# Kernel tuning notes

Hardware: AMD Instinct MI355X
Metric: run time of the kernel (lower is better)

## Reference

```python
import jax, jax.numpy as jnp
import numpy as np

T = 64          # temporal frames folded into batch: B = b * T
DIM = 64        # base_channel
V = 25          # num_point (skeleton joints)
NSTEP = 3       # n_step -> time_steps = arange(NSTEP+1)
CLIPS = 256     # b = N * M clips
B = CLIPS * T   # 16384
LEAK = 0.01     # nn.LeakyReLU default negative_slope


def _init_pe(length, d_model):
    # sinusoidal PE, identical to ODEFunc.init_pe
    pos = np.arange(length, dtype=np.float32)[:, None]
    div = np.exp(np.arange(0, d_model, 2, dtype=np.float32) * (-np.log(10000.0) / d_model))
    pe = np.zeros((length, d_model), dtype=np.float32)
    pe[:, 0::2] = np.sin(pos * div)
    pe[:, 1::2] = np.cos(pos * div)
    return jnp.asarray(pe)


def setup_inputs() -> dict:
    key = jax.random.key(0)
    ks = jax.random.split(key, 8)
    first_point = jax.random.normal(ks[0], (B, DIM, V), dtype=jnp.float32)
    # row-normalized random adjacency (stand-in for Graph.A_norm)
    A = jax.random.uniform(ks[1], (V, V), dtype=jnp.float32)
    A = A / jnp.sum(A, axis=1, keepdims=True)
    scale = 0.05
    W1 = jax.random.normal(ks[2], (DIM, DIM), dtype=jnp.float32) * scale
    b1 = jax.random.normal(ks[3], (DIM,), dtype=jnp.float32) * scale
    W2 = jax.random.normal(ks[4], (DIM, DIM), dtype=jnp.float32) * scale
    b2 = jax.random.normal(ks[5], (DIM,), dtype=jnp.float32) * scale
    Wp = jax.random.normal(ks[6], (DIM, DIM), dtype=jnp.float32) * scale
    bp = jax.random.normal(ks[7], (DIM,), dtype=jnp.float32) * scale
    temporal_pe = _init_pe(T + NSTEP, DIM)  # (T+N, dim) buffer
    time_steps = jnp.arange(NSTEP + 1, dtype=jnp.float32)
    return {"first_point": first_point, "time_steps": time_steps,
            "A": A, "W1": W1, "b1": b1, "W2": W2, "b2": b2,
            "Wp": Wp, "bp": bp, "temporal_pe": temporal_pe}


def reference(first_point, time_steps, A, W1, b1, W2, b2, Wp, bp, temporal_pe):
    Bn = first_point.shape[0]
    b = Bn // T

    def conv1x1(x, W, bb):  # Conv1d(dim, dim, 1): x (n, c, v)
        return jnp.einsum('oc,ncv->nov', W, x) + bb[None, :, None]

    def lrelu(x):
        return jnp.where(x >= 0, x, LEAK * x)

    def ode_func(t, x):
        # add_pe: pe rows [int(t), int(t)+T) added per-frame
        ti = jnp.floor(t).astype(jnp.int32)
        pe = jax.lax.dynamic_slice(temporal_pe, (ti, 0), (T, DIM))  # (T, dim)
        x = (x.reshape(b, T, DIM, V) + pe[None, :, :, None]).reshape(Bn, DIM, V)
        x = jnp.einsum('vu,ncu->ncv', A, x)
        x = lrelu(conv1x1(x, W1, b1))
        x = jnp.einsum('vu,ncu->ncv', A, x)
        x = lrelu(conv1x1(x, W2, b2))
        return conv1x1(x, Wp, bp)

    def rk4_step(y, t0_dt):  # torchdiffeq 'rk4' = 3/8-rule (rk4_alt_step_func)
        t0, dt = t0_dt
        k1 = ode_func(t0, y)
        k2 = ode_func(t0 + dt / 3, y + dt * k1 / 3)
        k3 = ode_func(t0 + 2 * dt / 3, y + dt * (k2 - k1 / 3))
        k4 = ode_func(t0 + dt, y + dt * (k1 - k2 + k3))
        y1 = y + dt * (k1 + 3 * (k2 + k3) + k4) / 8
        return y1, y1

    t0s = time_steps[:-1]
    dts = time_steps[1:] - time_steps[:-1]
    _, ys = jax.lax.scan(rk4_step, first_point, (t0s, dts))
    return jnp.concatenate([first_point[None], ys], axis=0)  # (NSTEP+1, B, C, V)
```

## Files before the change

kernel.cpp:

```cpp
#include <hip/hip_runtime.h>
#include <math.h>

#define DIMC 64
#define V25  25
#define NSTEP 3
#define BTOT 16384
#define LEAK 0.01f

typedef _Float16 half8  __attribute__((ext_vector_type(8)));
typedef _Float16 half4v __attribute__((ext_vector_type(4)));
typedef float    float4v __attribute__((ext_vector_type(4)));

#define MFMA16x16x32F16 __builtin_amdgcn_mfma_f32_16x16x32_f16

#define CV_STRIDE 36
#define VC_STRIDE 72
#define W_STRIDE  72

__device__ __forceinline__ int clampi03(int x) {
    return x < 0 ? 0 : (x > 3 ? 3 : x);
}

__launch_bounds__(256, 2)
__global__ void sode_kernel(const float* __restrict__ fp,
                            const float* __restrict__ ts,
                            const float* __restrict__ Ag,
                            const float* __restrict__ W1g, const float* __restrict__ b1g,
                            const float* __restrict__ W2g, const float* __restrict__ b2g,
                            const float* __restrict__ Wpg, const float* __restrict__ bpg,
                            const float* __restrict__ peg,
                            float* __restrict__ out)
{
    __shared__ __align__(16) _Float16 Wl[3*64*W_STRIDE];
    __shared__ __align__(16) _Float16 bufcv[4*64*CV_STRIDE];
    __shared__ __align__(16) _Float16 bufvc[4*32*VC_STRIDE];

    const int tid  = threadIdx.x;
    const int lane = tid & 63;
    const int wid  = tid >> 6;
    const int m    = lane & 15;
    const int q    = lane >> 4;
    const int n    = blockIdx.x * 4 + wid;
    const int tmod = n & 63;

    for (int idx = tid; idx < 64*64; idx += 256) {
        int o = idx >> 6, c = idx & 63;
        int d = o*W_STRIDE + c;
        Wl[d]                 = (_Float16)W1g[idx];
        Wl[64*W_STRIDE + d]   = (_Float16)W2g[idx];
        Wl[2*64*W_STRIDE + d] = (_Float16)Wpg[idx];
    }
    __syncthreads();

    _Float16* bcv = bufcv + wid * 64 * CV_STRIDE;
    _Float16* bvc = bufvc + wid * 32 * VC_STRIDE;

    half8 BA[2];
    for (int nt = 0; nt < 2; ++nt) {
        int v = 16*nt + m;
        for (int j = 0; j < 8; ++j) {
            int u = 8*q + j;
            BA[nt][j] = (v < V25 && u < V25) ? (_Float16)Ag[v*V25 + u] : (_Float16)0.f;
        }
    }

    float4v Y[4][2], Acc[4][2], D[4][2], kreg[4][2];
    for (int mt = 0; mt < 4; ++mt)
      for (int nt = 0; nt < 2; ++nt) {
        float4v y;
        int v = 16*nt + m;
        for (int r = 0; r < 4; ++r) {
            int c = 16*mt + 4*q + r;
            y[r] = (v < V25) ? fp[(size_t)n*1600 + c*25 + v] : 0.f;
        }
        Y[mt][nt] = y;
      }

    const float4v z4 = {0.f, 0.f, 0.f, 0.f};

    auto stage = [&](int ti, auto&& fxn) {
        const float* perow = peg + (ti + tmod) * 64;
        for (int mt = 0; mt < 4; ++mt) {
            float pv[4];
            for (int r = 0; r < 4; ++r) pv[r] = perow[16*mt + 4*q + r];
            for (int nt = 0; nt < 2; ++nt) {
                int v = 16*nt + m;
                for (int r = 0; r < 4; ++r)
                    bcv[(16*mt + 4*q + r)*CV_STRIDE + v] = (_Float16)(fxn(mt, nt, r) + pv[r]);
            }
        }
    };

    auto amix = [&]() {
        half8 af[4];
        for (int mt = 0; mt < 4; ++mt) {
            const half4v* p = (const half4v*)(bcv + (16*mt + m)*CV_STRIDE + 8*q);
            half4v lo = p[0], hi = p[1];
            half8 a;
            for (int j = 0; j < 4; ++j) { a[j] = lo[j]; a[4+j] = hi[j]; }
            af[mt] = a;
        }
        float4v acc[4][2];
        for (int mt = 0; mt < 4; ++mt)
          for (int nt = 0; nt < 2; ++nt)
            acc[mt][nt] = MFMA16x16x32F16(af[mt], BA[nt], z4, 0, 0, 0);
        for (int mt = 0; mt < 4; ++mt)
          for (int nt = 0; nt < 2; ++nt) {
            half4v h;
            for (int r = 0; r < 4; ++r) h[r] = (_Float16)acc[mt][nt][r];
            *(half4v*)(bvc + (16*nt + m)*VC_STRIDE + 16*mt + 4*q) = h;
          }
    };

    auto conv = [&](const _Float16* Wbase, const float* bias, bool act, int dst) {
        half8 bf[2][2];
        for (int nt = 0; nt < 2; ++nt)
          for (int ks = 0; ks < 2; ++ks)
            bf[nt][ks] = *(const half8*)(bvc + (16*nt + m)*VC_STRIDE + 32*ks + 8*q);
        float4v acc[4][2];
        for (int mt = 0; mt < 4; ++mt) {
            const _Float16* wr = Wbase + (16*mt + m)*W_STRIDE + 8*q;
            half8 w0 = *(const half8*)(wr);
            half8 w1 = *(const half8*)(wr + 32);
            for (int nt = 0; nt < 2; ++nt) {
                float4v a = MFMA16x16x32F16(w0, bf[nt][0], z4, 0, 0, 0);
                acc[mt][nt] = MFMA16x16x32F16(w1, bf[nt][1], a, 0, 0, 0);
            }
        }
        for (int mt = 0; mt < 4; ++mt) {
            float bv[4];
            for (int r = 0; r < 4; ++r) bv[r] = bias[16*mt + 4*q + r];
            for (int nt = 0; nt < 2; ++nt) {
                float4v a = acc[mt][nt];
                for (int r = 0; r < 4; ++r) {
                    float x = a[r] + bv[r];
                    if (act) x = (x >= 0.f) ? x : LEAK * x;
                    a[r] = x;
                }
                if (dst == 2) {
                    kreg[mt][nt] = a;
                } else if (dst == 1) {
                    half4v h;
                    for (int r = 0; r < 4; ++r) h[r] = (_Float16)a[r];
                    *(half4v*)(bvc + (16*nt + m)*VC_STRIDE + 16*mt + 4*q) = h;
                } else {
                    int v = 16*nt + m;
                    for (int r = 0; r < 4; ++r)
                        bcv[(16*mt + 4*q + r)*CV_STRIDE + v] = (_Float16)a[r];
                }
            }
        }
    };

    auto feval = [&]() {
        amix();
        conv(Wl,                 b1g, true,  0);
        amix();
        conv(Wl +   64*W_STRIDE, b2g, true,  1);
        conv(Wl + 2*64*W_STRIDE, bpg, false, 2);
    };

    auto store_Y = [&](int step) {
        float* op = out + (size_t)step * BTOT * 1600 + (size_t)n * 1600;
        for (int mt = 0; mt < 4; ++mt)
          for (int nt = 0; nt < 2; ++nt) {
            int v = 16*nt + m;
            if (v < V25)
                for (int r = 0; r < 4; ++r)
                    op[(16*mt + 4*q + r)*25 + v] = Y[mt][nt][r];
          }
    };

    store_Y(0);

    float tsr[4];
    for (int i = 0; i < 4; ++i) tsr[i] = ts[i];

#pragma unroll 1
    for (int st = 0; st < NSTEP; ++st) {
        float t0 = tsr[st];
        float dt = tsr[st+1] - t0;
        float dt3 = dt * (1.f/3.f);
        int ti1 = clampi03((int)floorf(t0));
        int ti2 = clampi03((int)floorf(t0 + dt3));
        int ti3 = clampi03((int)floorf(t0 + 2.f*dt3));
        int ti4 = clampi03((int)floorf(t0 + dt));

        stage(ti1, [&](int mt, int nt, int r) { return Y[mt][nt][r]; });
        feval();
        for (int mt = 0; mt < 4; ++mt)
          for (int nt = 0; nt < 2; ++nt) { Acc[mt][nt] = kreg[mt][nt]; D[mt][nt] = kreg[mt][nt]; }
        stage(ti2, [&](int mt, int nt, int r) { return Y[mt][nt][r] + dt3 * kreg[mt][nt][r]; });

        feval();
        stage(ti3, [&](int mt, int nt, int r) {
            return Y[mt][nt][r] + dt * kreg[mt][nt][r] - dt3 * Acc[mt][nt][r];
        });
        for (int mt = 0; mt < 4; ++mt)
          for (int nt = 0; nt < 2; ++nt)
            for (int r = 0; r < 4; ++r) {
                float kk = kreg[mt][nt][r];
                Acc[mt][nt][r] += 3.f * kk;
                D[mt][nt][r]   -= kk;
            }

        feval();
        stage(ti4, [&](int mt, int nt, int r) {
            return Y[mt][nt][r] + dt * (D[mt][nt][r] + kreg[mt][nt][r]);
        });
        for (int mt = 0; mt < 4; ++mt)
          for (int nt = 0; nt < 2; ++nt)
            for (int r = 0; r < 4; ++r)
                Acc[mt][nt][r] += 3.f * kreg[mt][nt][r];

        feval();
        for (int mt = 0; mt < 4; ++mt)
          for (int nt = 0; nt < 2; ++nt)
            for (int r = 0; r < 4; ++r)
                Y[mt][nt][r] += dt * 0.125f * (Acc[mt][nt][r] + kreg[mt][nt][r]);

        store_Y(st + 1);
    }
}

extern "C" void kernel_launch(void* const* d_in, const int* in_sizes, int n_in,
                              void* d_out, int out_size, void* d_ws, size_t ws_size,
                              hipStream_t stream) {
    const float* fp = (const float*)d_in[0];
    const float* ts = (const float*)d_in[1];
    const float* A  = (const float*)d_in[2];
    const float* W1 = (const float*)d_in[3];
    const float* b1 = (const float*)d_in[4];
    const float* W2 = (const float*)d_in[5];
    const float* b2 = (const float*)d_in[6];
    const float* Wp = (const float*)d_in[7];
    const float* bp = (const float*)d_in[8];
    const float* pe = (const float*)d_in[9];
    float* out = (float*)d_out;

    sode_kernel<<<dim3(BTOT/4), dim3(256), 0, stream>>>(fp, ts, A, W1, b1, W2, b2, Wp, bp, pe, out);
}
```

Baseline: 1.581 ms.

## Stage PE, biases in LDS; coalesce output stores; merge per-wave staging buffers

Caches the per-wave positional-encoding rows and the three bias vectors in shared memory and reads them as float4. The initial output copy becomes a block-wide vectorized memcpy, and later stores go through an LDS transpose so each wave writes contiguous float4 rows. The two per-wave staging buffers are merged into one region to cut LDS use, which relies on each stage finishing its reads before overwriting the shared space. The aim is fewer scattered global loads and stores per RK stage, plus higher occupancy from the smaller LDS footprint.

```diff
diff --git a/kernel.cpp b/kernel.cpp
--- a/kernel.cpp
+++ b/kernel.cpp
@@ -32,8 +32,9 @@
                             float* __restrict__ out)
 {
     __shared__ __align__(16) _Float16 Wl[3*64*W_STRIDE];
-    __shared__ __align__(16) _Float16 bufcv[4*64*CV_STRIDE];
-    __shared__ __align__(16) _Float16 bufvc[4*32*VC_STRIDE];
+    __shared__ __align__(16) _Float16 stg[4*2304];
+    __shared__ __align__(16) float    pel[4*256];
+    __shared__ __align__(16) float    bl[192];
 
     const int tid  = threadIdx.x;
     const int lane = tid & 63;
@@ -50,10 +51,24 @@
         Wl[64*W_STRIDE + d]   = (_Float16)W2g[idx];
         Wl[2*64*W_STRIDE + d] = (_Float16)Wpg[idx];
     }
+    for (int i = tid; i < 192; i += 256) {
+        int w = i >> 6, c = i & 63;
+        bl[i] = (w == 0) ? b1g[c] : (w == 1) ? b2g[c] : bpg[c];
+    }
+    float* pew = pel + wid * 256;
+    for (int i = lane; i < 256; i += 64)
+        pew[i] = peg[(tmod + (i >> 6)) * 64 + (i & 63)];
+
+    {
+        const float4v* src = (const float4v*)(fp + (size_t)blockIdx.x * 6400);
+        float4v*       dst = (float4v*)(out + (size_t)blockIdx.x * 6400);
+        for (int i = tid; i < 1600; i += 256) dst[i] = src[i];
+    }
+
     __syncthreads();
 
-    _Float16* bcv = bufcv + wid * 64 * CV_STRIDE;
-    _Float16* bvc = bufvc + wid * 32 * VC_STRIDE;
+    _Float16* bcv = stg + wid * 2304;
+    _Float16* bvc = stg + wid * 2304;
 
     half8 BA[2];
     for (int nt = 0; nt < 2; ++nt) {
@@ -79,10 +94,9 @@
     const float4v z4 = {0.f, 0.f, 0.f, 0.f};
 
     auto stage = [&](int ti, auto&& fxn) {
-        const float* perow = peg + (ti + tmod) * 64;
-        for (int mt = 0; mt < 4; ++mt) {
-            float pv[4];
-            for (int r = 0; r < 4; ++r) pv[r] = perow[16*mt + 4*q + r];
+        const float* perow = pew + ti * 64;
+        for (int mt = 0; mt < 4; ++mt) {
+            float4v pv = *(const float4v*)(perow + 16*mt + 4*q);
             for (int nt = 0; nt < 2; ++nt) {
                 int v = 16*nt + m;
                 for (int r = 0; r < 4; ++r)
@@ -128,8 +142,7 @@
             }
         }
         for (int mt = 0; mt < 4; ++mt) {
-            float bv[4];
-            for (int r = 0; r < 4; ++r) bv[r] = bias[16*mt + 4*q + r];
+            float4v bv = *(const float4v*)(bias + 16*mt + 4*q);
             for (int nt = 0; nt < 2; ++nt) {
                 float4v a = acc[mt][nt];
                 for (int r = 0; r < 4; ++r) {
@@ -154,24 +167,31 @@
 
     auto feval = [&]() {
         amix();
-        conv(Wl,                 b1g, true,  0);
+        conv(Wl,                 bl,       true,  0);
         amix();
-        conv(Wl +   64*W_STRIDE, b2g, true,  1);
-        conv(Wl + 2*64*W_STRIDE, bpg, false, 2);
+        conv(Wl +   64*W_STRIDE, bl + 64,  true,  1);
+        conv(Wl + 2*64*W_STRIDE, bl + 128, false, 2);
     };
 
     auto store_Y = [&](int step) {
         float* op = out + (size_t)step * BTOT * 1600 + (size_t)n * 1600;
-        for (int mt = 0; mt < 4; ++mt)
-          for (int nt = 0; nt < 2; ++nt) {
-            int v = 16*nt + m;
-            if (v < V25)
-                for (int r = 0; r < 4; ++r)
-                    op[(16*mt + 4*q + r)*25 + v] = Y[mt][nt][r];
-          }
-    };
-
-    store_Y(0);
+        float* sf = (float*)bcv;
+        for (int p = 0; p < 2; ++p) {
+            for (int mt = 2*p; mt < 2*p + 2; ++mt)
+              for (int nt = 0; nt < 2; ++nt) {
+                int v = 16*nt + m;
+                if (v < V25)
+                  for (int r = 0; r < 4; ++r) {
+                    int c = 16*mt + 4*q + r;
+                    sf[(c - 32*p)*25 + v] = Y[mt][nt][r];
+                  }
+              }
+            float4v* od = (float4v*)(op + p*800);
+            const float4v* sv = (const float4v*)sf;
+            for (int i = lane; i < 200; i += 64)
+                od[i] = sv[i];
+        }
+    };
 
     float tsr[4];
     for (int i = 0; i < 4; ++i) tsr[i] = ts[i];
```

Result: slower. 3.419 ms (+116.2%).
